# Optimization experiments

Measured on AMD Instinct MI355X. Metric: run time of the kernel, lower is better.

The kernel has to match this reference:

```python
import jax, jax.numpy as jnp
import numpy as np


def _qkernel(r, i, j, k):
    # Build the real-valued block kernel of a quaternion dense layer.
    # r,i,j,k: [in/4, out/4] -> kernel [in, out] implementing the Hamilton product.
    col_r = jnp.concatenate([r, -i, -j, -k], axis=0)
    col_i = jnp.concatenate([i, r, -k, j], axis=0)
    col_j = jnp.concatenate([j, k, r, -i], axis=0)
    col_k = jnp.concatenate([k, -j, i, r], axis=0)
    return jnp.concatenate([col_r, col_i, col_j, col_k], axis=1)


def setup_inputs() -> dict:
    key = jax.random.key(0)
    ks = jax.random.split(key, 12)
    B, F, H = 32768, 1024, 256
    F4, H4 = F // 4, H // 4
    s_in = 1.0 / np.sqrt(F)
    s_h = 1.0 / np.sqrt(H)
    inp = {
        "x": jax.random.normal(ks[0], (B, F), dtype=jnp.float32),
        "wx_r": jax.random.normal(ks[1], (4, F4, H4), dtype=jnp.float32) * s_in,
        "wx_i": jax.random.normal(ks[2], (4, F4, H4), dtype=jnp.float32) * s_in,
        "wx_j": jax.random.normal(ks[3], (4, F4, H4), dtype=jnp.float32) * s_in,
        "wx_k": jax.random.normal(ks[4], (4, F4, H4), dtype=jnp.float32) * s_in,
        "bx": jnp.zeros((4, H), dtype=jnp.float32),
        "uh_r": jax.random.normal(ks[5], (4, H4, H4), dtype=jnp.float32) * s_h,
        "uh_i": jax.random.normal(ks[6], (4, H4, H4), dtype=jnp.float32) * s_h,
        "uh_j": jax.random.normal(ks[7], (4, H4, H4), dtype=jnp.float32) * s_h,
        "uh_k": jax.random.normal(ks[8], (4, H4, H4), dtype=jnp.float32) * s_h,
        "fco_w": jax.random.normal(ks[9], (H, H), dtype=jnp.float32) * s_h,
        "fco_b": jnp.zeros((H,), dtype=jnp.float32),
    }
    return inp


def reference(x, wx_r, wx_i, wx_j, wx_k, bx, uh_r, uh_i, uh_j, uh_k, fco_w, fco_b):
    # Single-step quaternion LSTM cell with zero initial hidden/cell state.
    # Gate order along leading axis: [forget, input, output, cell].
    Kx = jax.vmap(_qkernel)(wx_r, wx_i, wx_j, wx_k)   # [4, F, H]
    Ku = jax.vmap(_qkernel)(uh_r, uh_i, uh_j, uh_k)   # [4, H, H]
    H = bx.shape[1]
    h0 = jnp.zeros((x.shape[0], H), dtype=x.dtype)
    c0 = h0
    gx = jnp.einsum('bf,gfh->gbh', x, Kx) + bx[:, None, :]   # [4, B, H]
    gu = jnp.einsum('bh,ghk->gbk', h0, Ku)                    # [4, B, H]
    z = gx + gu
    ft = jax.nn.sigmoid(z[0])
    it = jax.nn.sigmoid(z[1])
    ot = jax.nn.sigmoid(z[2])
    at = z[3]
    c = it * jnp.tanh(at) + ft * c0
    h = ot * jnp.tanh(c)
    return h @ fco_w + fco_b
```

## Files before the change

### kernel.cpp

```cpp
#include <hip/hip_runtime.h>
#include <cstdint>
#include <cstddef>

#define WS_WP   0
#define WS_FCO  1572864
#define WS_BP   1703936
#define WS_HVP  1707008

typedef __attribute__((ext_vector_type(8))) __bf16 bf16x8;
typedef __attribute__((ext_vector_type(4))) __bf16 bf16x4;
typedef __attribute__((ext_vector_type(4))) float floatx4;

__device__ __forceinline__ unsigned short f2bf(float f) {
  unsigned int u = __builtin_bit_cast(unsigned int, f);
  u += 0x7fffu + ((u >> 16) & 1u);
  return (unsigned short)(u >> 16);
}

__device__ __forceinline__ float sigmf(float z) {
  return __builtin_amdgcn_rcpf(1.f + __expf(-z));
}
__device__ __forceinline__ float tanh_(float z) {
  return 1.f - 2.f * __builtin_amdgcn_rcpf(1.f + __expf(2.f * z));
}

__device__ __forceinline__ void gld16(const void* g, void* l) {
  __builtin_amdgcn_global_load_lds(
      (const __attribute__((address_space(1))) unsigned int*)g,
      (__attribute__((address_space(3))) unsigned int*)l, 16, 0, 0);
}

__global__ __launch_bounds__(256) void pack_k(
    const float* __restrict__ wr, const float* __restrict__ wi,
    const float* __restrict__ wj, const float* __restrict__ wk,
    const float* __restrict__ bx, const float* __restrict__ fw,
    unsigned short* __restrict__ Wp, unsigned short* __restrict__ Fp,
    float* __restrict__ bp) {
  int t = threadIdx.x;
  if (blockIdx.x < 384) {
    int gpp = blockIdx.x >> 7;
    int oct = blockIdx.x & 127;
    int gp = gpp + 1;
    int h = t;
    int hb = h >> 6, hr = h & 63;
    int f0 = oct << 3;
    int fb = f0 >> 8, fr0 = f0 & 255;
    const int   comp_t[4][4] = {{0,1,2,3},{1,0,3,2},{2,3,0,1},{3,2,1,0}};
    const float sign_t[4][4] = {{1.f,-1.f,-1.f,-1.f},{1.f,1.f,-1.f,1.f},
                                {1.f,1.f,1.f,-1.f},{1.f,-1.f,1.f,1.f}};
    const float* srcs[4] = {wr, wi, wj, wk};
    const float* s = srcs[comp_t[hb][fb]] + ((size_t)((gp << 8) + fr0)) * 64 + hr;
    float sg = sign_t[hb][fb];
    unsigned short v[8];
#pragma unroll
    for (int j = 0; j < 8; ++j) v[j] = f2bf(sg * s[(size_t)j * 64]);
    int c = h * 3 + gpp;
    int cb = c / 192, nl = c % 192;
    int kb = oct >> 2, q = oct & 3;
    int idx16 = (nl << 2) + (q ^ ((nl >> 1) & 3));
    uint4 val = make_uint4(
        (unsigned)v[0] | ((unsigned)v[1] << 16), (unsigned)v[2] | ((unsigned)v[3] << 16),
        (unsigned)v[4] | ((unsigned)v[5] << 16), (unsigned)v[6] | ((unsigned)v[7] << 16));
    *(uint4*)(Wp + (size_t)(cb * 32 + kb) * 6144 + idx16 * 8) = val;
    if (oct == 0) bp[c] = bx[(gp << 8) + h];
  } else {
    int oct = blockIdx.x - 384;
    int n = t;
    int k0 = oct << 3;
    unsigned short v[8];
#pragma unroll
    for (int j = 0; j < 8; ++j) v[j] = f2bf(fw[(size_t)(k0 + j) * 256 + n]);
    int nb = n >> 7, nl = n & 127, kb = oct >> 2, q = oct & 3;
    int idx16 = (nl << 2) + (q ^ ((nl >> 1) & 3));
    uint4 val = make_uint4(
        (unsigned)v[0] | ((unsigned)v[1] << 16), (unsigned)v[2] | ((unsigned)v[3] << 16),
        (unsigned)v[4] | ((unsigned)v[5] << 16), (unsigned)v[6] | ((unsigned)v[7] << 16));
    *(uint4*)(Fp + (size_t)((nb << 3) + kb) * 4096 + idx16 * 8) = val;
  }
}

__global__ __launch_bounds__(256, 2) void gemm1_k(
    const float* __restrict__ x, const unsigned short* __restrict__ Wp,
    const float* __restrict__ bp, unsigned short* __restrict__ hvp) {
  __shared__ char smem[61440];
  float* zep = (float*)smem;

  const int t = threadIdx.x;
  const int lane = t & 63, wid = t >> 6;
  const int wm = wid >> 1, wn = wid & 1;
  const int lrow = lane & 15, q = lane >> 4;
  const int rowt = blockIdx.x;
  const int cby = blockIdx.y;
  const int row0 = rowt * 128;
  const float* xbase = x + (size_t)row0 * 1024;
  const unsigned short* wpb = Wp + (size_t)cby * 32 * 6144;

  const int sr = t >> 3, skq = t & 7;
  const int sq8 = skq >> 1, shalf = skq & 1;

  floatx4 acc[4][6];
#pragma unroll
  for (int i = 0; i < 4; ++i)
#pragma unroll
    for (int j = 0; j < 6; ++j) acc[i][j] = (floatx4){0.f, 0.f, 0.f, 0.f};

#define STAGE_B(bufi, kt)                                                     \
  {                                                                           \
    unsigned short* sBs_ = (unsigned short*)(smem + (bufi) * 20480 + 8192);   \
    const unsigned short* bt_ = wpb + (size_t)(kt) * 6144;                    \
    _Pragma("unroll")                                                         \
    for (int i_ = 0; i_ < 3; ++i_) {                                          \
      int s_ = t + i_ * 256;                                                  \
      gld16(bt_ + s_ * 8, sBs_ + s_ * 8);                                     \
    }                                                                         \
  }
#define LOAD_A(ra, kt)                                                        \
  {                                                                           \
    const float* ab_ = xbase + (kt) * 32 + skq * 4;                           \
    _Pragma("unroll")                                                         \
    for (int i_ = 0; i_ < 4; ++i_)                                            \
      ra[i_] = *(const float4*)(ab_ + (size_t)(i_ * 32 + sr) * 1024);         \
  }
#define WRITE_A(ra, bufi)                                                     \
  {                                                                           \
    unsigned short* sAs_ = (unsigned short*)(smem + (bufi) * 20480);          \
    _Pragma("unroll")                                                         \
    for (int i_ = 0; i_ < 4; ++i_) {                                          \
      int m_ = i_ * 32 + sr;                                                  \
      int slot_ = (m_ << 2) + (sq8 ^ ((m_ >> 1) & 3));                        \
      bf16x4 v_;                                                              \
      v_[0] = (__bf16)ra[i_].x; v_[1] = (__bf16)ra[i_].y;                     \
      v_[2] = (__bf16)ra[i_].z; v_[3] = (__bf16)ra[i_].w;                     \
      *(bf16x4*)(sAs_ + slot_ * 8 + shalf * 4) = v_;                          \
    }                                                                         \
  }
#define COMPUTE(bufi)                                                         \
  {                                                                           \
    const unsigned short* sA_ = (const unsigned short*)(smem + (bufi) * 20480);\
    const unsigned short* sB_ = sA_ + 4096;                                   \
    bf16x8 af[4], bf[6];                                                      \
    _Pragma("unroll")                                                         \
    for (int mt = 0; mt < 4; ++mt) {                                          \
      int m = wm * 64 + mt * 16 + lrow;                                       \
      int slot = (m << 2) + (q ^ ((m >> 1) & 3));                             \
      af[mt] = *(const bf16x8*)(const void*)(sA_ + slot * 8);                 \
    }                                                                         \
    _Pragma("unroll")                                                         \
    for (int nt = 0; nt < 6; ++nt) {                                          \
      int n = wn * 96 + nt * 16 + lrow;                                       \
      int off16 = (n << 2) + (q ^ ((n >> 1) & 3));                            \
      bf[nt] = *(const bf16x8*)(const void*)(sB_ + off16 * 8);                \
    }                                                                         \
    _Pragma("unroll")                                                         \
    for (int mt = 0; mt < 4; ++mt)                                            \
      _Pragma("unroll")                                                       \
      for (int nt = 0; nt < 6; ++nt)                                          \
        acc[mt][nt] = __builtin_amdgcn_mfma_f32_16x16x32_bf16(                \
            af[mt], bf[nt], acc[mt][nt], 0, 0, 0);                            \
  }
#define BODY(kt, RC, RN)                                                      \
  {                                                                           \
    if ((kt) < 30) {                                                          \
      LOAD_A(RN, (kt) + 2)                                                    \
      STAGE_B(((kt) + 2) % 3, (kt) + 2)                                       \
    }                                                                         \
    COMPUTE((kt) % 3)                                                         \
    if ((kt) < 30) {                                                          \
      asm volatile("s_waitcnt vmcnt(7)" ::: "memory");                        \
    } else {                                                                  \
      asm volatile("s_waitcnt vmcnt(0)" ::: "memory");                        \
    }                                                                         \
    if ((kt) < 31) { WRITE_A(RC, ((kt) + 1) % 3) }                            \
    asm volatile("s_waitcnt lgkmcnt(0)" ::: "memory");                        \
    __builtin_amdgcn_s_barrier();                                             \
    asm volatile("" ::: "memory");                                            \
  }

  float4 raA[4], raB[4];
  LOAD_A(raA, 0)
  STAGE_B(0, 0)
  LOAD_A(raB, 1)
  STAGE_B(1, 1)
  WRITE_A(raA, 0)
  asm volatile("s_waitcnt vmcnt(7)" ::: "memory");
  asm volatile("s_waitcnt lgkmcnt(0)" ::: "memory");
  __builtin_amdgcn_s_barrier();
  asm volatile("" ::: "memory");

  for (int kt2 = 0; kt2 < 32; kt2 += 2) {
    BODY(kt2, raB, raA)
    BODY(kt2 + 1, raA, raB)
  }
#undef BODY
#undef COMPUTE
#undef STAGE_B
#undef LOAD_A
#undef WRITE_A
  __syncthreads();

  const float* bp0 = bp + cby * 192;
  const int er = t >> 3, oc = t & 7;
#pragma unroll
  for (int pass = 0; pass < 4; ++pass) {
    if (wm == (pass >> 1)) {
      int mtb = (pass & 1) * 2;
#pragma unroll
      for (int mi = 0; mi < 2; ++mi)
#pragma unroll
        for (int nt = 0; nt < 6; ++nt)
#pragma unroll
          for (int r = 0; r < 4; ++r)
            zep[(mi * 16 + q * 4 + r) * 201 + wn * 96 + nt * 16 + lrow] = acc[mtb + mi][nt][r];
    }
    __syncthreads();
    {
      int ml = pass * 32 + er;
      unsigned short v[8];
#pragma unroll
      for (int j = 0; j < 8; ++j) {
        int hl = oc * 8 + j;
        float zi = zep[er * 201 + hl * 3 + 0] + bp0[hl * 3 + 0];
        float zo = zep[er * 201 + hl * 3 + 1] + bp0[hl * 3 + 1];
        float zc = zep[er * 201 + hl * 3 + 2] + bp0[hl * 3 + 2];
        float it = sigmf(zi);
        float ot = sigmf(zo);
        float cc = it * tanh_(zc);
        v[j] = f2bf(ot * tanh_(cc));
      }
      int ktile = cby * 2 + (oc >> 2), qq = oc & 3;
      int idx16 = (ml << 2) + (qq ^ ((ml >> 1) & 3));
      uint4 val = make_uint4(
          (unsigned)v[0] | ((unsigned)v[1] << 16), (unsigned)v[2] | ((unsigned)v[3] << 16),
          (unsigned)v[4] | ((unsigned)v[5] << 16), (unsigned)v[6] | ((unsigned)v[7] << 16));
      *(uint4*)(hvp + (size_t)(rowt * 8 + ktile) * 4096 + idx16 * 8) = val;
    }
    __syncthreads();
  }
}

__global__ __launch_bounds__(256, 4) void gemm2_k(
    const unsigned short* __restrict__ hvp, const unsigned short* __restrict__ Fp,
    const float* __restrict__ fcob, float* __restrict__ out) {
  __shared__ unsigned short sB[32768];
  const int t = threadIdx.x;
  const int lane = t & 63, wid = t >> 6;
  const int wm = wid >> 1, wn = wid & 1;
  const int lrow = lane & 15, q = lane >> 4;
  const int mb = blockIdx.x, nb = blockIdx.y;

  const unsigned short* fpb = Fp + (size_t)nb * 32768;
#pragma unroll
  for (int i = 0; i < 16; ++i) gld16(fpb + (t + i * 256) * 8, sB + (t + i * 256) * 8);

  floatx4 acc[4][4];
#pragma unroll
  for (int i = 0; i < 4; ++i)
#pragma unroll
    for (int j = 0; j < 4; ++j) acc[i][j] = (floatx4){0.f, 0.f, 0.f, 0.f};
  __syncthreads();

#pragma unroll
  for (int kt = 0; kt < 8; ++kt) {
    const unsigned short* at_ = hvp + (size_t)(mb * 8 + kt) * 4096;
    bf16x8 af[4], bf[4];
#pragma unroll
    for (int mt = 0; mt < 4; ++mt) {
      int m = wm * 64 + mt * 16 + lrow;
      int o = (m << 2) + (q ^ ((m >> 1) & 3));
      af[mt] = *(const bf16x8*)(const void*)(at_ + o * 8);
    }
#pragma unroll
    for (int nt = 0; nt < 4; ++nt) {
      int n = wn * 64 + nt * 16 + lrow;
      int o = (n << 2) + (q ^ ((n >> 1) & 3));
      bf[nt] = *(const bf16x8*)(const void*)(sB + kt * 4096 + o * 8);
    }
#pragma unroll
    for (int mt = 0; mt < 4; ++mt)
#pragma unroll
      for (int nt = 0; nt < 4; ++nt)
        acc[mt][nt] = __builtin_amdgcn_mfma_f32_16x16x32_bf16(af[mt], bf[nt], acc[mt][nt], 0, 0, 0);
  }
#pragma unroll
  for (int nt = 0; nt < 4; ++nt) {
    int colg = nb * 128 + wn * 64 + nt * 16 + lrow;
    float bias = fcob[colg];
#pragma unroll
    for (int mt = 0; mt < 4; ++mt) {
      int rowg = mb * 128 + wm * 64 + mt * 16 + q * 4;
#pragma unroll
      for (int r = 0; r < 4; ++r)
        out[(size_t)(rowg + r) * 256 + colg] = acc[mt][nt][r] + bias;
    }
  }
}

extern "C" void kernel_launch(void* const* d_in, const int* in_sizes, int n_in,
                              void* d_out, int out_size, void* d_ws, size_t ws_size,
                              hipStream_t stream) {
  const float* x  = (const float*)d_in[0];
  const float* wr = (const float*)d_in[1];
  const float* wi = (const float*)d_in[2];
  const float* wj = (const float*)d_in[3];
  const float* wk = (const float*)d_in[4];
  const float* bx = (const float*)d_in[5];
  const float* fw = (const float*)d_in[10];
  const float* fb = (const float*)d_in[11];
  char* ws = (char*)d_ws;
  unsigned short* Wp  = (unsigned short*)(ws + WS_WP);
  unsigned short* Fp  = (unsigned short*)(ws + WS_FCO);
  float*          bp  = (float*)(ws + WS_BP);
  unsigned short* hvp = (unsigned short*)(ws + WS_HVP);
  float*          out = (float*)d_out;

  hipLaunchKernelGGL(pack_k,  dim3(416),    dim3(256), 0, stream, wr, wi, wj, wk, bx, fw, Wp, Fp, bp);
  hipLaunchKernelGGL(gemm1_k, dim3(256, 4), dim3(256), 0, stream, x, Wp, bp, hvp);
  hipLaunchKernelGGL(gemm2_k, dim3(256, 2), dim3(256), 0, stream, hvp, Fp, fb, out);
}
```

Baseline: 287.8 us.

## Widen gemm1 tile to two column blocks with 512-thread workgroups

Each gemm1 workgroup now computes a 128x384 output tile, covering two packed weight column blocks, using 8 waves instead of 4. The grid shrinks from 4 to 2 column blocks, so each row of x is loaded from global memory and converted to bf16 half as often. LDS use rises to 96KB per block, which likely allows only one block per CU. Overall wave occupancy stays about the same, but there are fewer independent blocks to hide barrier stalls.

```diff
diff --git a/kernel.cpp b/kernel.cpp
--- a/kernel.cpp
+++ b/kernel.cpp
@@ -79,24 +79,24 @@
   }
 }
 
-__global__ __launch_bounds__(256, 2) void gemm1_k(
+__global__ __launch_bounds__(512, 2) void gemm1_k(
     const float* __restrict__ x, const unsigned short* __restrict__ Wp,
     const float* __restrict__ bp, unsigned short* __restrict__ hvp) {
-  __shared__ char smem[61440];
+  __shared__ char smem[98304];
   float* zep = (float*)smem;
 
   const int t = threadIdx.x;
   const int lane = t & 63, wid = t >> 6;
-  const int wm = wid >> 1, wn = wid & 1;
+  const int wm = wid >> 2, wn = wid & 3;
   const int lrow = lane & 15, q = lane >> 4;
   const int rowt = blockIdx.x;
-  const int cby = blockIdx.y;
+  const int nbq = blockIdx.y;
+  const int cb0 = nbq * 2;
   const int row0 = rowt * 128;
   const float* xbase = x + (size_t)row0 * 1024;
-  const unsigned short* wpb = Wp + (size_t)cby * 32 * 6144;
-
-  const int sr = t >> 3, skq = t & 7;
-  const int sq8 = skq >> 1, shalf = skq & 1;
+
+  const int m0 = t >> 3, kq = t & 7;
+  const int sq8 = kq >> 1, shalf = kq & 1;
 
   floatx4 acc[4][6];
 #pragma unroll
@@ -106,27 +106,29 @@
 
 #define STAGE_B(bufi, kt)                                                     \
   {                                                                           \
-    unsigned short* sBs_ = (unsigned short*)(smem + (bufi) * 20480 + 8192);   \
-    const unsigned short* bt_ = wpb + (size_t)(kt) * 6144;                    \
+    unsigned short* sBs_ = (unsigned short*)(smem + (bufi) * 32768 + 8192);   \
+    const unsigned short* bt0_ = Wp + ((size_t)cb0 * 32 + (kt)) * 6144;       \
     _Pragma("unroll")                                                         \
     for (int i_ = 0; i_ < 3; ++i_) {                                          \
-      int s_ = t + i_ * 256;                                                  \
-      gld16(bt_ + s_ * 8, sBs_ + s_ * 8);                                     \
+      int s_ = t + i_ * 512;                                                  \
+      int cbL_ = s_ >= 768;                                                   \
+      const unsigned short* src_ =                                            \
+          bt0_ + (size_t)cbL_ * 196608 + (s_ - cbL_ * 768) * 8;               \
+      gld16(src_, sBs_ + s_ * 8);                                             \
     }                                                                         \
   }
 #define LOAD_A(ra, kt)                                                        \
   {                                                                           \
-    const float* ab_ = xbase + (kt) * 32 + skq * 4;                           \
-    _Pragma("unroll")                                                         \
-    for (int i_ = 0; i_ < 4; ++i_)                                            \
-      ra[i_] = *(const float4*)(ab_ + (size_t)(i_ * 32 + sr) * 1024);         \
+    const float* ab_ = xbase + (size_t)m0 * 1024 + (kt) * 32 + kq * 4;        \
+    ra[0] = *(const float4*)(ab_);                                            \
+    ra[1] = *(const float4*)(ab_ + 64 * 1024);                                \
   }
 #define WRITE_A(ra, bufi)                                                     \
   {                                                                           \
-    unsigned short* sAs_ = (unsigned short*)(smem + (bufi) * 20480);          \
-    _Pragma("unroll")                                                         \
-    for (int i_ = 0; i_ < 4; ++i_) {                                          \
-      int m_ = i_ * 32 + sr;                                                  \
+    unsigned short* sAs_ = (unsigned short*)(smem + (bufi) * 32768);          \
+    _Pragma("unroll")                                                         \
+    for (int i_ = 0; i_ < 2; ++i_) {                                          \
+      int m_ = m0 + i_ * 64;                                                  \
       int slot_ = (m_ << 2) + (sq8 ^ ((m_ >> 1) & 3));                        \
       bf16x4 v_;                                                              \
       v_[0] = (__bf16)ra[i_].x; v_[1] = (__bf16)ra[i_].y;                     \
@@ -136,7 +138,7 @@
   }
 #define COMPUTE(bufi)                                                         \
   {                                                                           \
-    const unsigned short* sA_ = (const unsigned short*)(smem + (bufi) * 20480);\
+    const unsigned short* sA_ = (const unsigned short*)(smem + (bufi) * 32768);\
     const unsigned short* sB_ = sA_ + 4096;                                   \
     bf16x8 af[4], bf[6];                                                      \
     _Pragma("unroll")                                                         \
@@ -147,9 +149,10 @@
     }                                                                         \
     _Pragma("unroll")                                                         \
     for (int nt = 0; nt < 6; ++nt) {                                          \
-      int n = wn * 96 + nt * 16 + lrow;                                       \
-      int off16 = (n << 2) + (q ^ ((n >> 1) & 3));                            \
-      bf[nt] = *(const bf16x8*)(const void*)(sB_ + off16 * 8);                \
+      int nl = (wn & 1) * 96 + nt * 16 + lrow;                                \
+      int off16 = (nl << 2) + (q ^ ((nl >> 1) & 3));                          \
+      bf[nt] = *(const bf16x8*)(const void*)(                                 \
+          sB_ + ((size_t)(wn >> 1) * 768 + off16) * 8);                       \
     }                                                                         \
     _Pragma("unroll")                                                         \
     for (int mt = 0; mt < 4; ++mt)                                            \
@@ -166,7 +169,7 @@
     }                                                                         \
     COMPUTE((kt) % 3)                                                         \
     if ((kt) < 30) {                                                          \
-      asm volatile("s_waitcnt vmcnt(7)" ::: "memory");                        \
+      asm volatile("s_waitcnt vmcnt(5)" ::: "memory");                        \
     } else {                                                                  \
       asm volatile("s_waitcnt vmcnt(0)" ::: "memory");                        \
     }                                                                         \
@@ -176,13 +179,13 @@
     asm volatile("" ::: "memory");                                            \
   }
 
-  float4 raA[4], raB[4];
+  float4 raA[2], raB[2];
   LOAD_A(raA, 0)
   STAGE_B(0, 0)
   LOAD_A(raB, 1)
   STAGE_B(1, 1)
   WRITE_A(raA, 0)
-  asm volatile("s_waitcnt vmcnt(7)" ::: "memory");
+  asm volatile("s_waitcnt vmcnt(5)" ::: "memory");
   asm volatile("s_waitcnt lgkmcnt(0)" ::: "memory");
   __builtin_amdgcn_s_barrier();
   asm volatile("" ::: "memory");
@@ -198,8 +201,9 @@
 #undef WRITE_A
   __syncthreads();
 
-  const float* bp0 = bp + cby * 192;
-  const int er = t >> 3, oc = t & 7;
+  const float* bp0 = bp + cb0 * 192;
+  const int er = t >> 4, oc = t & 15;
+  const int cbL = oc >> 3, oo = oc & 7;
 #pragma unroll
   for (int pass = 0; pass < 4; ++pass) {
     if (wm == (pass >> 1)) {
@@ -210,7 +214,7 @@
         for (int nt = 0; nt < 6; ++nt)
 #pragma unroll
           for (int r = 0; r < 4; ++r)
-            zep[(mi * 16 + q * 4 + r) * 201 + wn * 96 + nt * 16 + lrow] = acc[mtb + mi][nt][r];
+            zep[(mi * 16 + q * 4 + r) * 385 + wn * 96 + nt * 16 + lrow] = acc[mtb + mi][nt][r];
     }
     __syncthreads();
     {
@@ -218,16 +222,17 @@
       unsigned short v[8];
 #pragma unroll
       for (int j = 0; j < 8; ++j) {
-        int hl = oc * 8 + j;
-        float zi = zep[er * 201 + hl * 3 + 0] + bp0[hl * 3 + 0];
-        float zo = zep[er * 201 + hl * 3 + 1] + bp0[hl * 3 + 1];
-        float zc = zep[er * 201 + hl * 3 + 2] + bp0[hl * 3 + 2];
+        int hl = oo * 8 + j;
+        int cz = cbL * 192 + hl * 3;
+        float zi = zep[er * 385 + cz + 0] + bp0[cz + 0];
+        float zo = zep[er * 385 + cz + 1] + bp0[cz + 1];
+        float zc = zep[er * 385 + cz + 2] + bp0[cz + 2];
         float it = sigmf(zi);
         float ot = sigmf(zo);
         float cc = it * tanh_(zc);
         v[j] = f2bf(ot * tanh_(cc));
       }
-      int ktile = cby * 2 + (oc >> 2), qq = oc & 3;
+      int ktile = (cb0 + cbL) * 2 + (oo >> 2), qq = oo & 3;
       int idx16 = (ml << 2) + (qq ^ ((ml >> 1) & 3));
       uint4 val = make_uint4(
           (unsigned)v[0] | ((unsigned)v[1] << 16), (unsigned)v[2] | ((unsigned)v[3] << 16),
@@ -314,6 +319,6 @@
   float*          out = (float*)d_out;
 
   hipLaunchKernelGGL(pack_k,  dim3(416),    dim3(256), 0, stream, wr, wi, wj, wk, bx, fw, Wp, Fp, bp);
-  hipLaunchKernelGGL(gemm1_k, dim3(256, 4), dim3(256), 0, stream, x, Wp, bp, hvp);
+  hipLaunchKernelGGL(gemm1_k, dim3(256, 2), dim3(512), 0, stream, x, Wp, bp, hvp);
   hipLaunchKernelGGL(gemm2_k, dim3(256, 2), dim3(256), 0, stream, hvp, Fp, fb, out);
 }
```

Result: no change. 291.0 us (+1.1%).

## Load GEMM1 A fragments directly to registers and prefetch GEMM2 A tiles

Applied to the files above, without the earlier changes.

The first GEMM no longer stages the fp32 x tile through LDS. Each lane loads exactly the 8 k-values it needs for its MFMA A fragment straight from global memory and converts them to bf16 in registers. This removes the LDS writes, the LDS reads and the A-side swizzle, and shrinks shared memory, which could raise occupancy. The cost is more register pressure and less coalesced global loads, since each lane reads 32 bytes per row across 4 row groups. The second GEMM also software-prefetches the next k-tile's A fragments from global memory into registers.

```diff
diff --git a/kernel.cpp b/kernel.cpp
--- a/kernel.cpp
+++ b/kernel.cpp
@@ -8,7 +8,6 @@
 #define WS_HVP  1707008
 
 typedef __attribute__((ext_vector_type(8))) __bf16 bf16x8;
-typedef __attribute__((ext_vector_type(4))) __bf16 bf16x4;
 typedef __attribute__((ext_vector_type(4))) float floatx4;
 
 __device__ __forceinline__ unsigned short f2bf(float f) {
@@ -82,7 +81,7 @@
 __global__ __launch_bounds__(256, 2) void gemm1_k(
     const float* __restrict__ x, const unsigned short* __restrict__ Wp,
     const float* __restrict__ bp, unsigned short* __restrict__ hvp) {
-  __shared__ char smem[61440];
+  __shared__ char smem[36864];
   float* zep = (float*)smem;
 
   const int t = threadIdx.x;
@@ -91,60 +90,52 @@
   const int lrow = lane & 15, q = lane >> 4;
   const int rowt = blockIdx.x;
   const int cby = blockIdx.y;
-  const int row0 = rowt * 128;
-  const float* xbase = x + (size_t)row0 * 1024;
+  const float* xfrag = x + (size_t)(rowt * 128 + wm * 64 + lrow) * 1024 + q * 8;
   const unsigned short* wpb = Wp + (size_t)cby * 32 * 6144;
 
-  const int sr = t >> 3, skq = t & 7;
-  const int sq8 = skq >> 1, shalf = skq & 1;
-
   floatx4 acc[4][6];
 #pragma unroll
   for (int i = 0; i < 4; ++i)
 #pragma unroll
     for (int j = 0; j < 6; ++j) acc[i][j] = (floatx4){0.f, 0.f, 0.f, 0.f};
 
+  bf16x8 afc[4];
+
 #define STAGE_B(bufi, kt)                                                     \
   {                                                                           \
-    unsigned short* sBs_ = (unsigned short*)(smem + (bufi) * 20480 + 8192);   \
+    unsigned short* sB_ = (unsigned short*)(smem + (bufi) * 12288);           \
     const unsigned short* bt_ = wpb + (size_t)(kt) * 6144;                    \
     _Pragma("unroll")                                                         \
     for (int i_ = 0; i_ < 3; ++i_) {                                          \
       int s_ = t + i_ * 256;                                                  \
-      gld16(bt_ + s_ * 8, sBs_ + s_ * 8);                                     \
-    }                                                                         \
-  }
-#define LOAD_A(ra, kt)                                                        \
-  {                                                                           \
-    const float* ab_ = xbase + (kt) * 32 + skq * 4;                           \
-    _Pragma("unroll")                                                         \
-    for (int i_ = 0; i_ < 4; ++i_)                                            \
-      ra[i_] = *(const float4*)(ab_ + (size_t)(i_ * 32 + sr) * 1024);         \
-  }
-#define WRITE_A(ra, bufi)                                                     \
-  {                                                                           \
-    unsigned short* sAs_ = (unsigned short*)(smem + (bufi) * 20480);          \
-    _Pragma("unroll")                                                         \
-    for (int i_ = 0; i_ < 4; ++i_) {                                          \
-      int m_ = i_ * 32 + sr;                                                  \
-      int slot_ = (m_ << 2) + (sq8 ^ ((m_ >> 1) & 3));                        \
-      bf16x4 v_;                                                              \
-      v_[0] = (__bf16)ra[i_].x; v_[1] = (__bf16)ra[i_].y;                     \
-      v_[2] = (__bf16)ra[i_].z; v_[3] = (__bf16)ra[i_].w;                     \
-      *(bf16x4*)(sAs_ + slot_ * 8 + shalf * 4) = v_;                          \
+      gld16(bt_ + s_ * 8, sB_ + s_ * 8);                                      \
+    }                                                                         \
+  }
+#define LOAD_A(R, kt)                                                         \
+  {                                                                           \
+    const float* p_ = xfrag + (kt) * 32;                                      \
+    _Pragma("unroll")                                                         \
+    for (int mt_ = 0; mt_ < 4; ++mt_) {                                       \
+      R[2 * mt_]     = *(const float4*)(p_ + mt_ * 16384);                    \
+      R[2 * mt_ + 1] = *(const float4*)(p_ + mt_ * 16384 + 4);                \
+    }                                                                         \
+  }
+#define CVT_A(R)                                                              \
+  {                                                                           \
+    _Pragma("unroll")                                                         \
+    for (int mt_ = 0; mt_ < 4; ++mt_) {                                       \
+      bf16x8 v_;                                                              \
+      v_[0] = (__bf16)R[2 * mt_].x;     v_[1] = (__bf16)R[2 * mt_].y;         \
+      v_[2] = (__bf16)R[2 * mt_].z;     v_[3] = (__bf16)R[2 * mt_].w;         \
+      v_[4] = (__bf16)R[2 * mt_ + 1].x; v_[5] = (__bf16)R[2 * mt_ + 1].y;     \
+      v_[6] = (__bf16)R[2 * mt_ + 1].z; v_[7] = (__bf16)R[2 * mt_ + 1].w;     \
+      afc[mt_] = v_;                                                          \
     }                                                                         \
   }
 #define COMPUTE(bufi)                                                         \
   {                                                                           \
-    const unsigned short* sA_ = (const unsigned short*)(smem + (bufi) * 20480);\
-    const unsigned short* sB_ = sA_ + 4096;                                   \
-    bf16x8 af[4], bf[6];                                                      \
-    _Pragma("unroll")                                                         \
-    for (int mt = 0; mt < 4; ++mt) {                                          \
-      int m = wm * 64 + mt * 16 + lrow;                                       \
-      int slot = (m << 2) + (q ^ ((m >> 1) & 3));                             \
-      af[mt] = *(const bf16x8*)(const void*)(sA_ + slot * 8);                 \
-    }                                                                         \
+    const unsigned short* sB_ = (const unsigned short*)(smem + (bufi) * 12288);\
+    bf16x8 bf[6];                                                             \
     _Pragma("unroll")                                                         \
     for (int nt = 0; nt < 6; ++nt) {                                          \
       int n = wn * 96 + nt * 16 + lrow;                                       \
@@ -156,34 +147,33 @@
       _Pragma("unroll")                                                       \
       for (int nt = 0; nt < 6; ++nt)                                          \
         acc[mt][nt] = __builtin_amdgcn_mfma_f32_16x16x32_bf16(                \
-            af[mt], bf[nt], acc[mt][nt], 0, 0, 0);                            \
+            afc[mt], bf[nt], acc[mt][nt], 0, 0, 0);                           \
   }
 #define BODY(kt, RC, RN)                                                      \
   {                                                                           \
-    if ((kt) < 30) {                                                          \
+    if ((kt) <= 29) {                                                         \
       LOAD_A(RN, (kt) + 2)                                                    \
       STAGE_B(((kt) + 2) % 3, (kt) + 2)                                       \
     }                                                                         \
     COMPUTE((kt) % 3)                                                         \
-    if ((kt) < 30) {                                                          \
-      asm volatile("s_waitcnt vmcnt(7)" ::: "memory");                        \
-    } else {                                                                  \
+    if ((kt) <= 29) {                                                         \
+      asm volatile("s_waitcnt vmcnt(11)" ::: "memory");                       \
+    } else if ((kt) == 30) {                                                  \
       asm volatile("s_waitcnt vmcnt(0)" ::: "memory");                        \
     }                                                                         \
-    if ((kt) < 31) { WRITE_A(RC, ((kt) + 1) % 3) }                            \
+    if ((kt) <= 30) { CVT_A(RC) }                                             \
     asm volatile("s_waitcnt lgkmcnt(0)" ::: "memory");                        \
     __builtin_amdgcn_s_barrier();                                             \
     asm volatile("" ::: "memory");                                            \
   }
 
-  float4 raA[4], raB[4];
+  float4 raA[8], raB[8];
   LOAD_A(raA, 0)
   STAGE_B(0, 0)
   LOAD_A(raB, 1)
   STAGE_B(1, 1)
-  WRITE_A(raA, 0)
-  asm volatile("s_waitcnt vmcnt(7)" ::: "memory");
-  asm volatile("s_waitcnt lgkmcnt(0)" ::: "memory");
+  asm volatile("s_waitcnt vmcnt(11)" ::: "memory");
+  CVT_A(raA)
   __builtin_amdgcn_s_barrier();
   asm volatile("" ::: "memory");
 
@@ -193,9 +183,9 @@
   }
 #undef BODY
 #undef COMPUTE
+#undef CVT_A
+#undef LOAD_A
 #undef STAGE_B
-#undef LOAD_A
-#undef WRITE_A
   __syncthreads();
 
   const float* bp0 = bp + cby * 192;
@@ -257,18 +247,32 @@
   for (int i = 0; i < 4; ++i)
 #pragma unroll
     for (int j = 0; j < 4; ++j) acc[i][j] = (floatx4){0.f, 0.f, 0.f, 0.f};
+
+  int aoff[4];
+#pragma unroll
+  for (int mt = 0; mt < 4; ++mt) {
+    int m = wm * 64 + mt * 16 + lrow;
+    aoff[mt] = ((m << 2) + (q ^ ((m >> 1) & 3))) * 8;
+  }
+  bf16x8 afc[4];
+  {
+    const unsigned short* at_ = hvp + (size_t)(mb * 8) * 4096;
+#pragma unroll
+    for (int mt = 0; mt < 4; ++mt)
+      afc[mt] = *(const bf16x8*)(const void*)(at_ + aoff[mt]);
+  }
   __syncthreads();
 
 #pragma unroll
   for (int kt = 0; kt < 8; ++kt) {
-    const unsigned short* at_ = hvp + (size_t)(mb * 8 + kt) * 4096;
-    bf16x8 af[4], bf[4];
-#pragma unroll
-    for (int mt = 0; mt < 4; ++mt) {
-      int m = wm * 64 + mt * 16 + lrow;
-      int o = (m << 2) + (q ^ ((m >> 1) & 3));
-      af[mt] = *(const bf16x8*)(const void*)(at_ + o * 8);
-    }
+    bf16x8 afn[4];
+    if (kt < 7) {
+      const unsigned short* at_ = hvp + (size_t)(mb * 8 + kt + 1) * 4096;
+#pragma unroll
+      for (int mt = 0; mt < 4; ++mt)
+        afn[mt] = *(const bf16x8*)(const void*)(at_ + aoff[mt]);
+    }
+    bf16x8 bf[4];
 #pragma unroll
     for (int nt = 0; nt < 4; ++nt) {
       int n = wn * 64 + nt * 16 + lrow;
@@ -279,7 +283,11 @@
     for (int mt = 0; mt < 4; ++mt)
 #pragma unroll
       for (int nt = 0; nt < 4; ++nt)
-        acc[mt][nt] = __builtin_amdgcn_mfma_f32_16x16x32_bf16(af[mt], bf[nt], acc[mt][nt], 0, 0, 0);
+        acc[mt][nt] = __builtin_amdgcn_mfma_f32_16x16x32_bf16(afc[mt], bf[nt], acc[mt][nt], 0, 0, 0);
+    if (kt < 7) {
+#pragma unroll
+      for (int mt = 0; mt < 4; ++mt) afc[mt] = afn[mt];
+    }
   }
 #pragma unroll
   for (int nt = 0; nt < 4; ++nt) {
```

Result: slower. 342.7 us (+19.1%).
